# Kernel optimization log

Measured on AMD Instinct MI355X. Metric: run time of the kernel, lower is better.

## Reference

```python
import jax, jax.numpy as jnp
import numpy as np

B, S, D = 8, 2048, 512
EPS = 1e-6
ROPE_THETA = 10000.0


def setup_inputs() -> dict:
    key = jax.random.key(0)
    ks = jax.random.split(key, 8)
    scale = 0.02
    return {
        "x": jax.random.normal(ks[0], (B, S, D), dtype=jnp.float32),
        "conv_w": jax.random.normal(ks[1], (D, D, 3), dtype=jnp.float32) * scale,
        "conv_b": jnp.zeros((D,), dtype=jnp.float32),
        "pre_g": jnp.ones((D,), dtype=jnp.float32),
        "q_g": jnp.ones((D,), dtype=jnp.float32),
        "k_g": jnp.ones((D,), dtype=jnp.float32),
        "Wq": jax.random.normal(ks[2], (D, D), dtype=jnp.float32) * scale,
        "Wk": jax.random.normal(ks[3], (D, D), dtype=jnp.float32) * scale,
        "Wv": jax.random.normal(ks[4], (D, D), dtype=jnp.float32) * scale,
    }


def _rmsnorm(x, g, eps=EPS):
    ms = jnp.mean(jnp.square(x), axis=-1, keepdims=True)
    return x * jax.lax.rsqrt(ms + eps) * g


def _rope_tables(seq_len, head_dim, dtype=jnp.float32):
    inv = 1.0 / (ROPE_THETA ** (jnp.arange(0, head_dim, 2, dtype=dtype) / head_dim))
    freqs = jnp.arange(seq_len, dtype=dtype)[:, None] * inv[None, :]  # [S, D/2]
    return jnp.cos(freqs), jnp.sin(freqs)


def _apply_rope(x, cos, sin):
    # x: [B, S, D]; treat last dim as D/2 complex pairs (interleaved real/imag)
    b, s, d = x.shape
    xr = x.reshape(b, s, d // 2, 2)
    x0, x1 = xr[..., 0], xr[..., 1]
    c = cos[None, :, :]
    sn = sin[None, :, :]
    o0 = x0 * c - x1 * sn
    o1 = x0 * sn + x1 * c
    return jnp.stack([o0, o1], axis=-1).reshape(b, s, d)


def reference(x, conv_w, conv_b, pre_g, q_g, k_g, Wq, Wk, Wv):
    b, s, d = x.shape
    # Conv1d over sequence axis (kernel 3, padding 1)
    xc = jnp.transpose(x, (0, 2, 1))  # [B, D, S]
    xc = jax.lax.conv_general_dilated(
        xc, conv_w, window_strides=(1,), padding=[(1, 1)],
        dimension_numbers=("NCH", "OIH", "NCH"))
    xc = xc + conv_b[None, :, None]
    x_norm = _rmsnorm(jnp.transpose(xc, (0, 2, 1)), pre_g)  # [B, S, D]

    q = _rmsnorm(jnp.einsum("bsd,ed->bse", x_norm, Wq), q_g)
    k = _rmsnorm(jnp.einsum("bsd,ed->bse", x_norm, Wk), k_g)
    v = jnp.einsum("bsd,ed->bse", x_norm, Wv)

    cos, sin = _rope_tables(s, d, x.dtype)
    q = _apply_rope(q, cos, sin)
    k = _apply_rope(k, cos, sin)

    scores = jnp.einsum("bqd,bkd->bqk", q, k) / jnp.sqrt(jnp.asarray(d, x.dtype))
    w = jax.nn.softmax(scores, axis=-1)  # dropout is identity in eval mode
    attended = jnp.einsum("bqk,bkd->bqd", w, v)
    out = x + attended
    return out.mean(axis=1)  # [B, D]
```

## Files before the change

kernel.cpp:

```cpp
#include <hip/hip_runtime.h>
#include <math.h>

#define BB 8
#define SS 2048
#define DDIM 512
#define KC 1536
#define EPSV 1e-6f
#define SCALE 0.044194173824159216f
#define LDP  40
#define LDP2 72

typedef unsigned short ushort_t;
using short8 = __attribute__((ext_vector_type(8))) short;
using f32x4  = __attribute__((ext_vector_type(4))) float;

__device__ inline unsigned short f2bf(float f) {
    union { float f; unsigned int u; } v; v.f = f;
    unsigned int r = v.u + 0x7FFFu + ((v.u >> 16) & 1u);
    return (unsigned short)(r >> 16);
}
__device__ inline unsigned int packbf(float a, float b) {
    return (unsigned int)f2bf(a) | ((unsigned int)f2bf(b) << 16);
}
__device__ inline float bf2f(unsigned short s) {
    union { unsigned int u; float f; } v; v.u = ((unsigned int)s) << 16; return v.f;
}
__device__ inline short8 ldfrag(const ushort_t* s, int row, int ko) {
    return *reinterpret_cast<const short8*>(&s[row * LDP + ko]);
}
__device__ inline short8 ldfrag2(const ushort_t* s, int row, int ko) {
    return *reinterpret_cast<const short8*>(&s[row * LDP2 + ko]);
}
__device__ inline uint4 lda_bc(const ushort_t* Ag, int s_, int ko) {
    return (s_ >= 0 && s_ < SS) ? *reinterpret_cast<const uint4*>(&Ag[(size_t)s_ * DDIM + ko])
                                : make_uint4(0, 0, 0, 0);
}

__global__ __launch_bounds__(256) void kx_cast(const float* __restrict__ x,
                                               ushort_t* __restrict__ xbf,
                                               float* __restrict__ xsum)
{
    const int t = threadIdx.x;
    const int b = blockIdx.y;
    const int r0 = blockIdx.x * 16;
    const int c0 = 2 * t;
    float s0 = 0.f, s1 = 0.f;
    for (int r = 0; r < 16; r++) {
        size_t row = (size_t)b * SS + r0 + r;
        float2 v = *reinterpret_cast<const float2*>(&x[row * DDIM + c0]);
        s0 += v.x; s1 += v.y;
        *reinterpret_cast<unsigned int*>(&xbf[row * DDIM + c0]) = packbf(v.x, v.y);
    }
    atomicAdd(&xsum[b * DDIM + c0], s0);
    atomicAdd(&xsum[b * DDIM + c0 + 1], s1);
}

__global__ __launch_bounds__(256) void k0_prep(
    const float* __restrict__ conv_w, const float* __restrict__ Wq,
    const float* __restrict__ Wk, const float* __restrict__ Wv,
    ushort_t* __restrict__ wcat, ushort_t* __restrict__ wqkv)
{
    int idx = blockIdx.x * 256 + threadIdx.x;
    {
        int o = idx / KC, kk = idx - o * KC;
        int t = kk >> 9, i = kk & 511;
        wcat[idx] = f2bf(conv_w[(size_t)o * KC + i * 3 + t]);
    }
    {
        int n = idx >> 9, d = idx & 511;
        const float* src = (n < 512) ? &Wq[(size_t)n * DDIM + d]
                         : (n < 1024) ? &Wk[(size_t)(n - 512) * DDIM + d]
                         : &Wv[(size_t)(n - 1024) * DDIM + d];
        wqkv[idx] = f2bf(*src);
    }
}

__global__ __launch_bounds__(256) void k1b_conv(
    const ushort_t* __restrict__ xbf, const ushort_t* __restrict__ wcat,
    const float* __restrict__ conv_b, ushort_t* __restrict__ ybf, float* __restrict__ rs)
{
    __shared__ ushort_t As[128 * LDP2];
    __shared__ ushort_t Bs[128 * LDP2];
    const int t = threadIdx.x;
    const int lane = t & 63, w = t >> 6;
    const int lm = lane & 15, lq = lane >> 4;
    const int wm = w >> 1, wn = w & 1;
    const int sr = t >> 3, sc = (t & 7) * 8;
    const int s0 = blockIdx.x * 128;
    const int n0 = blockIdx.y * 128;
    const int b  = blockIdx.z;
    const ushort_t* Ag = xbf + (size_t)b * SS * DDIM;
    const ushort_t* Bg = wcat + (size_t)n0 * KC;

    f32x4 acc[4][4];
    #pragma unroll
    for (int i = 0; i < 4; i++)
        #pragma unroll
        for (int j = 0; j < 4; j++) acc[i][j] = (f32x4){0.f, 0.f, 0.f, 0.f};

    uint4 ra0, ra1, ra2, ra3, rb0, rb1, rb2, rb3;
    #define LOADAB(dc) { \
        int tg_ = (dc) >> 3, ko_ = ((dc) & 7) * 64 + sc, kb_ = (dc) * 64 + sc; \
        int sa_ = s0 + sr + tg_ - 1; \
        ra0 = lda_bc(Ag, sa_,      ko_); ra1 = lda_bc(Ag, sa_ + 32, ko_); \
        ra2 = lda_bc(Ag, sa_ + 64, ko_); ra3 = lda_bc(Ag, sa_ + 96, ko_); \
        rb0 = *reinterpret_cast<const uint4*>(&Bg[(size_t)sr * KC + kb_]); \
        rb1 = *reinterpret_cast<const uint4*>(&Bg[(size_t)(sr + 32) * KC + kb_]); \
        rb2 = *reinterpret_cast<const uint4*>(&Bg[(size_t)(sr + 64) * KC + kb_]); \
        rb3 = *reinterpret_cast<const uint4*>(&Bg[(size_t)(sr + 96) * KC + kb_]); }

    LOADAB(0);
    for (int dc = 0; dc < 24; dc++) {
        *reinterpret_cast<uint4*>(&As[(sr)      * LDP2 + sc]) = ra0;
        *reinterpret_cast<uint4*>(&As[(sr + 32) * LDP2 + sc]) = ra1;
        *reinterpret_cast<uint4*>(&As[(sr + 64) * LDP2 + sc]) = ra2;
        *reinterpret_cast<uint4*>(&As[(sr + 96) * LDP2 + sc]) = ra3;
        *reinterpret_cast<uint4*>(&Bs[(sr)      * LDP2 + sc]) = rb0;
        *reinterpret_cast<uint4*>(&Bs[(sr + 32) * LDP2 + sc]) = rb1;
        *reinterpret_cast<uint4*>(&Bs[(sr + 64) * LDP2 + sc]) = rb2;
        *reinterpret_cast<uint4*>(&Bs[(sr + 96) * LDP2 + sc]) = rb3;
        __syncthreads();
        if (dc < 23) LOADAB(dc + 1);
        #pragma unroll
        for (int half = 0; half < 2; half++) {
            short8 af0 = ldfrag2(As, wm * 64 +  0 + lm, half * 32 + lq * 8);
            short8 af1 = ldfrag2(As, wm * 64 + 16 + lm, half * 32 + lq * 8);
            short8 af2 = ldfrag2(As, wm * 64 + 32 + lm, half * 32 + lq * 8);
            short8 af3 = ldfrag2(As, wm * 64 + 48 + lm, half * 32 + lq * 8);
            #pragma unroll
            for (int nt = 0; nt < 4; nt++) {
                short8 bfv = ldfrag2(Bs, wn * 64 + nt * 16 + lm, half * 32 + lq * 8);
                acc[0][nt] = __builtin_amdgcn_mfma_f32_16x16x32_bf16(af0, bfv, acc[0][nt], 0, 0, 0);
                acc[1][nt] = __builtin_amdgcn_mfma_f32_16x16x32_bf16(af1, bfv, acc[1][nt], 0, 0, 0);
                acc[2][nt] = __builtin_amdgcn_mfma_f32_16x16x32_bf16(af2, bfv, acc[2][nt], 0, 0, 0);
                acc[3][nt] = __builtin_amdgcn_mfma_f32_16x16x32_bf16(af3, bfv, acc[3][nt], 0, 0, 0);
            }
        }
        __syncthreads();
    }
    #undef LOADAB

    const int rbase = s0 + wm * 64;
    const int cbase = n0 + wn * 64;
    ushort_t* yb = ybf + (size_t)b * SS * DDIM;
    float* rsb = rs + (size_t)b * SS;
    float bias[4];
    #pragma unroll
    for (int nt = 0; nt < 4; nt++) bias[nt] = conv_b[cbase + nt * 16 + lm];
    #pragma unroll
    for (int mt = 0; mt < 4; mt++) {
        float pr[4] = {0.f, 0.f, 0.f, 0.f};
        #pragma unroll
        for (int nt = 0; nt < 4; nt++) {
            #pragma unroll
            for (int r = 0; r < 4; r++) {
                float val = acc[mt][nt][r] + bias[nt];
                yb[(size_t)(rbase + mt * 16 + lq * 4 + r) * DDIM + cbase + nt * 16 + lm] = f2bf(val);
                pr[r] = fmaf(val, val, pr[r]);
            }
        }
        #pragma unroll
        for (int r = 0; r < 4; r++) {
            float p = pr[r];
            p += __shfl_xor(p, 1, 64); p += __shfl_xor(p, 2, 64);
            p += __shfl_xor(p, 4, 64); p += __shfl_xor(p, 8, 64);
            if (lm == 0) atomicAdd(&rsb[rbase + mt * 16 + lq * 4 + r], p);
        }
    }
}

__global__ __launch_bounds__(256) void k1n_norm(
    const ushort_t* __restrict__ ybf, const float* __restrict__ rs,
    const float* __restrict__ pre_g, ushort_t* __restrict__ xnbf)
{
    const int t = threadIdx.x;
    const int b = blockIdx.y;
    const int r0 = blockIdx.x * 8;
    float2 pg = *reinterpret_cast<const float2*>(&pre_g[2 * t]);
    for (int r = 0; r < 8; r++) {
        size_t row = (size_t)b * SS + r0 + r;
        float inv = rsqrtf(rs[row] * (1.0f / DDIM) + EPSV);
        unsigned int yv = *reinterpret_cast<const unsigned int*>(&ybf[row * DDIM + 2 * t]);
        float v0 = bf2f((ushort_t)(yv & 0xFFFF)), v1 = bf2f((ushort_t)(yv >> 16));
        *reinterpret_cast<unsigned int*>(&xnbf[row * DDIM + 2 * t]) =
            packbf(v0 * inv * pg.x, v1 * inv * pg.y);
    }
}

__global__ __launch_bounds__(256) void k1c_qkv(
    const ushort_t* __restrict__ xnbf, const ushort_t* __restrict__ wqkv,
    ushort_t* __restrict__ qraw, ushort_t* __restrict__ kraw, ushort_t* __restrict__ vb,
    float* __restrict__ rq, float* __restrict__ rk)
{
    __shared__ ushort_t As[128 * LDP2];
    __shared__ ushort_t Bs[128 * LDP2];
    const int t = threadIdx.x;
    const int lane = t & 63, w = t >> 6;
    const int lm = lane & 15, lq = lane >> 4;
    const int wm = w >> 1, wn = w & 1;
    const int sr = t >> 3, sc = (t & 7) * 8;
    const int s0 = blockIdx.x * 128;
    const int n0 = blockIdx.y * 128;
    const int b  = blockIdx.z;
    const ushort_t* Ag = xnbf + ((size_t)b * SS + s0) * DDIM;
    const ushort_t* Bg = wqkv + (size_t)n0 * DDIM;

    f32x4 acc[4][4];
    #pragma unroll
    for (int i = 0; i < 4; i++)
        #pragma unroll
        for (int j = 0; j < 4; j++) acc[i][j] = (f32x4){0.f, 0.f, 0.f, 0.f};

    uint4 ra0, ra1, ra2, ra3, rb0, rb1, rb2, rb3;
    #define LOADAB2(dc) { \
        int ko_ = (dc) * 64 + sc; \
        ra0 = *reinterpret_cast<const uint4*>(&Ag[(size_t)sr * DDIM + ko_]); \
        ra1 = *reinterpret_cast<const uint4*>(&Ag[(size_t)(sr + 32) * DDIM + ko_]); \
        ra2 = *reinterpret_cast<const uint4*>(&Ag[(size_t)(sr + 64) * DDIM + ko_]); \
        ra3 = *reinterpret_cast<const uint4*>(&Ag[(size_t)(sr + 96) * DDIM + ko_]); \
        rb0 = *reinterpret_cast<const uint4*>(&Bg[(size_t)sr * DDIM + ko_]); \
        rb1 = *reinterpret_cast<const uint4*>(&Bg[(size_t)(sr + 32) * DDIM + ko_]); \
        rb2 = *reinterpret_cast<const uint4*>(&Bg[(size_t)(sr + 64) * DDIM + ko_]); \
        rb3 = *reinterpret_cast<const uint4*>(&Bg[(size_t)(sr + 96) * DDIM + ko_]); }

    LOADAB2(0);
    for (int dc = 0; dc < 8; dc++) {
        *reinterpret_cast<uint4*>(&As[(sr)      * LDP2 + sc]) = ra0;
        *reinterpret_cast<uint4*>(&As[(sr + 32) * LDP2 + sc]) = ra1;
        *reinterpret_cast<uint4*>(&As[(sr + 64) * LDP2 + sc]) = ra2;
        *reinterpret_cast<uint4*>(&As[(sr + 96) * LDP2 + sc]) = ra3;
        *reinterpret_cast<uint4*>(&Bs[(sr)      * LDP2 + sc]) = rb0;
        *reinterpret_cast<uint4*>(&Bs[(sr + 32) * LDP2 + sc]) = rb1;
        *reinterpret_cast<uint4*>(&Bs[(sr + 64) * LDP2 + sc]) = rb2;
        *reinterpret_cast<uint4*>(&Bs[(sr + 96) * LDP2 + sc]) = rb3;
        __syncthreads();
        if (dc < 7) LOADAB2(dc + 1);
        #pragma unroll
        for (int half = 0; half < 2; half++) {
            short8 af0 = ldfrag2(As, wm * 64 +  0 + lm, half * 32 + lq * 8);
            short8 af1 = ldfrag2(As, wm * 64 + 16 + lm, half * 32 + lq * 8);
            short8 af2 = ldfrag2(As, wm * 64 + 32 + lm, half * 32 + lq * 8);
            short8 af3 = ldfrag2(As, wm * 64 + 48 + lm, half * 32 + lq * 8);
            #pragma unroll
            for (int nt = 0; nt < 4; nt++) {
                short8 bfv = ldfrag2(Bs, wn * 64 + nt * 16 + lm, half * 32 + lq * 8);
                acc[0][nt] = __builtin_amdgcn_mfma_f32_16x16x32_bf16(af0, bfv, acc[0][nt], 0, 0, 0);
                acc[1][nt] = __builtin_amdgcn_mfma_f32_16x16x32_bf16(af1, bfv, acc[1][nt], 0, 0, 0);
                acc[2][nt] = __builtin_amdgcn_mfma_f32_16x16x32_bf16(af2, bfv, acc[2][nt], 0, 0, 0);
                acc[3][nt] = __builtin_amdgcn_mfma_f32_16x16x32_bf16(af3, bfv, acc[3][nt], 0, 0, 0);
            }
        }
        __syncthreads();
    }
    #undef LOADAB2

    const int which = blockIdx.y >> 2;
    const int rbase = s0 + wm * 64;
    const int cbase = ((blockIdx.y & 3) * 128) + wn * 64;
    if (which == 2) {
        ushort_t* vbb = vb + (size_t)b * SS * DDIM;
        #pragma unroll
        for (int mt = 0; mt < 4; mt++)
            #pragma unroll
            for (int nt = 0; nt < 4; nt++)
                #pragma unroll
                for (int r = 0; r < 4; r++)
                    vbb[(size_t)(rbase + mt * 16 + lq * 4 + r) * DDIM + cbase + nt * 16 + lm] =
                        f2bf(acc[mt][nt][r]);
    } else {
        ushort_t* db = (which ? kraw : qraw) + (size_t)b * SS * DDIM;
        float* rb = (which ? rk : rq) + (size_t)b * SS;
        #pragma unroll
        for (int mt = 0; mt < 4; mt++) {
            float pr[4] = {0.f, 0.f, 0.f, 0.f};
            #pragma unroll
            for (int nt = 0; nt < 4; nt++) {
                #pragma unroll
                for (int r = 0; r < 4; r++) {
                    float val = acc[mt][nt][r];
                    db[(size_t)(rbase + mt * 16 + lq * 4 + r) * DDIM + cbase + nt * 16 + lm] = f2bf(val);
                    pr[r] = fmaf(val, val, pr[r]);
                }
            }
            #pragma unroll
            for (int r = 0; r < 4; r++) {
                float p = pr[r];
                p += __shfl_xor(p, 1, 64); p += __shfl_xor(p, 2, 64);
                p += __shfl_xor(p, 4, 64); p += __shfl_xor(p, 8, 64);
                if (lm == 0) atomicAdd(&rb[rbase + mt * 16 + lq * 4 + r], p);
            }
        }
    }
}

__global__ __launch_bounds__(256) void k1d_rope(
    ushort_t* q_io, ushort_t* k_io,
    const float* __restrict__ rq, const float* __restrict__ rk,
    const float* __restrict__ q_g, const float* __restrict__ k_g)
{
    const int t = threadIdx.x;
    const int b = blockIdx.y;
    const int r0 = blockIdx.x * 8;
    const int c0 = 2 * t;
    float qg0 = q_g[c0], qg1 = q_g[c0 + 1];
    float kg0 = k_g[c0], kg1 = k_g[c0 + 1];
    float invf = (float)pow(10000.0, -(double)c0 / (double)DDIM);
    for (int r = 0; r < 8; r++) {
        int srow = r0 + r;
        size_t rowi = (size_t)b * SS + srow;
        float iq = rsqrtf(rq[rowi] * (1.0f / DDIM) + EPSV);
        float ik = rsqrtf(rk[rowi] * (1.0f / DDIM) + EPSV);
        size_t off = rowi * DDIM + c0;
        unsigned int qv = *reinterpret_cast<const unsigned int*>(&q_io[off]);
        unsigned int kv = *reinterpret_cast<const unsigned int*>(&k_io[off]);
        float q0 = bf2f((ushort_t)(qv & 0xFFFF)) * iq * qg0;
        float q1 = bf2f((ushort_t)(qv >> 16)) * iq * qg1;
        float k0v = bf2f((ushort_t)(kv & 0xFFFF)) * ik * kg0;
        float k1v = bf2f((ushort_t)(kv >> 16)) * ik * kg1;
        float ang = (float)srow * invf, sn, cs;
        sincosf(ang, &sn, &cs);
        *reinterpret_cast<unsigned int*>(&q_io[off]) = packbf(q0 * cs - q1 * sn, q0 * sn + q1 * cs);
        *reinterpret_cast<unsigned int*>(&k_io[off]) = packbf(k0v * cs - k1v * sn, k0v * sn + k1v * cs);
    }
}

__global__ __launch_bounds__(256, 4) void k2a_rowsum(
    const ushort_t* __restrict__ qb, const ushort_t* __restrict__ kb,
    ushort_t* __restrict__ P, float* __restrict__ l)
{
    __shared__ ushort_t As[128 * LDP];
    __shared__ ushort_t Bs[128 * LDP];
    const int t = threadIdx.x;
    const int lane = t & 63, w = t >> 6;
    const int lm = lane & 15, lq = lane >> 4;
    const int wm = w >> 1, wn = w & 1;
    const int srow = t >> 2, scol = (t & 3) * 8;
    const int b  = blockIdx.x;
    const int qt = blockIdx.y;
    const int kt = blockIdx.z;

    const ushort_t* Ag = qb + ((size_t)b * SS + qt * 128) * DDIM;
    const ushort_t* Bg = kb + ((size_t)b * SS + kt * 128) * DDIM;

    f32x4 acc[4][4];
    #pragma unroll
    for (int i = 0; i < 4; i++)
        #pragma unroll
        for (int j = 0; j < 4; j++) acc[i][j] = (f32x4){0.f, 0.f, 0.f, 0.f};

    uint4 ra0 = *reinterpret_cast<const uint4*>(&Ag[(size_t)srow * DDIM + scol]);
    uint4 ra1 = *reinterpret_cast<const uint4*>(&Ag[(size_t)(srow + 64) * DDIM + scol]);
    uint4 rb0 = *reinterpret_cast<const uint4*>(&Bg[(size_t)srow * DDIM + scol]);
    uint4 rb1 = *reinterpret_cast<const uint4*>(&Bg[(size_t)(srow + 64) * DDIM + scol]);

    for (int dc = 0; dc < 16; dc++) {
        *reinterpret_cast<uint4*>(&As[srow * LDP + scol]) = ra0;
        *reinterpret_cast<uint4*>(&As[(srow + 64) * LDP + scol]) = ra1;
        *reinterpret_cast<uint4*>(&Bs[srow * LDP + scol]) = rb0;
        *reinterpret_cast<uint4*>(&Bs[(srow + 64) * LDP + scol]) = rb1;
        __syncthreads();
        if (dc < 15) {
            int off = (dc + 1) * 32 + scol;
            ra0 = *reinterpret_cast<const uint4*>(&Ag[(size_t)srow * DDIM + off]);
            ra1 = *reinterpret_cast<const uint4*>(&Ag[(size_t)(srow + 64) * DDIM + off]);
            rb0 = *reinterpret_cast<const uint4*>(&Bg[(size_t)srow * DDIM + off]);
            rb1 = *reinterpret_cast<const uint4*>(&Bg[(size_t)(srow + 64) * DDIM + off]);
        }
        short8 af[4];
        #pragma unroll
        for (int mt = 0; mt < 4; mt++)
            af[mt] = ldfrag(As, wm * 64 + mt * 16 + lm, lq * 8);
        #pragma unroll
        for (int nt = 0; nt < 4; nt++) {
            short8 bfv = ldfrag(Bs, wn * 64 + nt * 16 + lm, lq * 8);
            #pragma unroll
            for (int mt = 0; mt < 4; mt++)
                acc[mt][nt] = __builtin_amdgcn_mfma_f32_16x16x32_bf16(af[mt], bfv, acc[mt][nt], 0, 0, 0);
        }
        __syncthreads();
    }

    const int rbase = qt * 128 + wm * 64;
    const int cbase = kt * 128 + wn * 64;
    ushort_t* Pb = P + (size_t)b * SS * SS;
    float* lrow = l + (size_t)b * SS;
    #pragma unroll
    for (int mt = 0; mt < 4; mt++) {
        #pragma unroll
        for (int r = 0; r < 4; r++) {
            const int row = rbase + mt * 16 + lq * 4 + r;
            float rowp = 0.f;
            #pragma unroll
            for (int nt = 0; nt < 4; nt++) {
                float e = __expf(acc[mt][nt][r] * SCALE);
                Pb[(size_t)row * SS + cbase + nt * 16 + lm] = f2bf(e);
                rowp += e;
            }
            float p = rowp;
            p += __shfl_xor(p, 1, 64); p += __shfl_xor(p, 2, 64);
            p += __shfl_xor(p, 4, 64); p += __shfl_xor(p, 8, 64);
            if (lm == 0) atomicAdd(&lrow[row], p);
        }
    }
}

__global__ __launch_bounds__(256) void k2c_colred(
    const ushort_t* __restrict__ P, const float* __restrict__ l,
    float* __restrict__ cw)
{
    const int t = threadIdx.x;
    const int b = blockIdx.z;
    const int k0 = blockIdx.x * 1024 + t * 4;
    const int q0 = blockIdx.y * 128;
    const ushort_t* Pb = P + ((size_t)b * SS + q0) * SS;
    const float* lb = l + (size_t)b * SS + q0;
    float a0 = 0.f, a1 = 0.f, a2 = 0.f, a3 = 0.f;
    for (int q = 0; q < 128; q++) {
        float rl = 1.0f / lb[q];
        uint2 pp = *reinterpret_cast<const uint2*>(&Pb[(size_t)q * SS + k0]);
        a0 = fmaf(bf2f((ushort_t)(pp.x & 0xFFFF)), rl, a0);
        a1 = fmaf(bf2f((ushort_t)(pp.x >> 16)), rl, a1);
        a2 = fmaf(bf2f((ushort_t)(pp.y & 0xFFFF)), rl, a2);
        a3 = fmaf(bf2f((ushort_t)(pp.y >> 16)), rl, a3);
    }
    atomicAdd(&cw[(size_t)b * SS + k0], a0);
    atomicAdd(&cw[(size_t)b * SS + k0 + 1], a1);
    atomicAdd(&cw[(size_t)b * SS + k0 + 2], a2);
    atomicAdd(&cw[(size_t)b * SS + k0 + 3], a3);
}

__global__ __launch_bounds__(256) void k4_out(
    const float* __restrict__ xsum, const ushort_t* __restrict__ v,
    const float* __restrict__ cwv, float* __restrict__ out)
{
    const int b = blockIdx.x, c = blockIdx.y;
    const int t = threadIdx.x;
    const int srow0 = c * (SS / 16);
    const ushort_t* vb = v + ((size_t)b * SS + srow0) * DDIM;
    const float* cwb   = cwv + (size_t)b * SS + srow0;
    float a0 = (c == 0) ? xsum[b * DDIM + t]       : 0.f;
    float a1 = (c == 0) ? xsum[b * DDIM + t + 256] : 0.f;
    for (int r = 0; r < SS / 16; r++) {
        float w = cwb[r];
        a0 += w * bf2f(vb[(size_t)r * DDIM + t]);
        a1 += w * bf2f(vb[(size_t)r * DDIM + t + 256]);
    }
    atomicAdd(&out[b * DDIM + t],       a0 * (1.0f / SS));
    atomicAdd(&out[b * DDIM + t + 256], a1 * (1.0f / SS));
}

extern "C" void kernel_launch(void* const* d_in, const int* in_sizes, int n_in,
                              void* d_out, int out_size, void* d_ws, size_t ws_size,
                              hipStream_t stream)
{
    const float* x      = (const float*)d_in[0];
    const float* conv_w = (const float*)d_in[1];
    const float* conv_b = (const float*)d_in[2];
    const float* pre_g  = (const float*)d_in[3];
    const float* q_g    = (const float*)d_in[4];
    const float* k_g    = (const float*)d_in[5];
    const float* Wq     = (const float*)d_in[6];
    const float* Wk     = (const float*)d_in[7];
    const float* Wv     = (const float*)d_in[8];
    float* out          = (float*)d_out;

    const size_t NTOK = (size_t)BB * SS * DDIM;
    char* p = (char*)d_ws;
    ushort_t* xbf = (ushort_t*)p; p += NTOK * 2;
    ushort_t* ybf = (ushort_t*)p; p += NTOK * 2;
    ushort_t* xn  = (ushort_t*)p; p += NTOK * 2;
                         p += NTOK * 2;
    ushort_t* qio = (ushort_t*)p; p += NTOK * 2;
    ushort_t* kio = (ushort_t*)p; p += NTOK * 2;
    ushort_t* vb  = (ushort_t*)p; p += NTOK * 2;
    ushort_t* wcat = (ushort_t*)p; p += (size_t)DDIM * KC * 2;
    ushort_t* wqkv = (ushort_t*)p; p += (size_t)KC * DDIM * 2;
    float* rs   = (float*)p; p += (size_t)BB * SS * 4;
    float* rq   = (float*)p; p += (size_t)BB * SS * 4;
    float* rk   = (float*)p; p += (size_t)BB * SS * 4;
    float* lbuf = (float*)p; p += (size_t)BB * SS * 4;
    float* cwb  = (float*)p; p += (size_t)BB * SS * 4;
    float* xsum = (float*)p; p += (size_t)BB * DDIM * 4;

    ushort_t* Pbuf = xbf;

    (void)hipMemsetAsync(d_out, 0, (size_t)out_size * sizeof(float), stream);
    (void)hipMemsetAsync(rs, 0, ((size_t)BB * SS * 5 + (size_t)BB * DDIM) * sizeof(float), stream);

    kx_cast<<<dim3(SS / 16, BB), 256, 0, stream>>>(x, xbf, xsum);
    k0_prep<<<dim3(DDIM * KC / 256), 256, 0, stream>>>(conv_w, Wq, Wk, Wv, wcat, wqkv);
    k1b_conv<<<dim3(SS / 128, 4, BB), 256, 0, stream>>>(xbf, wcat, conv_b, ybf, rs);
    k1n_norm<<<dim3(SS / 8, BB), 256, 0, stream>>>(ybf, rs, pre_g, xn);
    k1c_qkv<<<dim3(SS / 128, 12, BB), 256, 0, stream>>>(xn, wqkv, qio, kio, vb, rq, rk);
    k1d_rope<<<dim3(SS / 8, BB), 256, 0, stream>>>(qio, kio, rq, rk, q_g, k_g);
    k2a_rowsum<<<dim3(BB, SS / 128, SS / 128), 256, 0, stream>>>(qio, kio, Pbuf, lbuf);
    k2c_colred<<<dim3(SS / 1024, SS / 128, BB), 256, 0, stream>>>(Pbuf, lbuf, cwb);
    k4_out<<<dim3(BB, 16), 256, 0, stream>>>(xsum, vb, cwb, out);
}
```

Measured before the change: 287.4 us.

## Use direct global-to-LDS loads with XOR-swizzled shared tiles in GEMM kernels

The conv, QKV and score GEMM kernels now move tiles straight from global memory into LDS with global_load_lds, replacing the register staging and padded LDS rows. The LDS layout is XOR-swizzled to avoid bank conflicts without padding. The bf16 copy of x gets zero halo rows, so the conv's shifted-row loads need no bounds checks and map onto one contiguous address. The score kernel also widens its K step to 64 and drops its occupancy launch hint. The aim is to cut register pressure and staging instructions, but the register prefetch that overlapped loads with MFMA work is gone, so each iteration now waits on its loads.

```diff
diff --git a/kernel.cpp b/kernel.cpp
--- a/kernel.cpp
+++ b/kernel.cpp
@@ -3,12 +3,11 @@
 
 #define BB 8
 #define SS 2048
+#define SSG 2050
 #define DDIM 512
 #define KC 1536
 #define EPSV 1e-6f
 #define SCALE 0.044194173824159216f
-#define LDP  40
-#define LDP2 72
 
 typedef unsigned short ushort_t;
 using short8 = __attribute__((ext_vector_type(8))) short;
@@ -25,15 +24,15 @@
 __device__ inline float bf2f(unsigned short s) {
     union { unsigned int u; float f; } v; v.u = ((unsigned int)s) << 16; return v.f;
 }
-__device__ inline short8 ldfrag(const ushort_t* s, int row, int ko) {
-    return *reinterpret_cast<const short8*>(&s[row * LDP + ko]);
-}
-__device__ inline short8 ldfrag2(const ushort_t* s, int row, int ko) {
-    return *reinterpret_cast<const short8*>(&s[row * LDP2 + ko]);
-}
-__device__ inline uint4 lda_bc(const ushort_t* Ag, int s_, int ko) {
-    return (s_ >= 0 && s_ < SS) ? *reinterpret_cast<const uint4*>(&Ag[(size_t)s_ * DDIM + ko])
-                                : make_uint4(0, 0, 0, 0);
+
+__device__ inline void gload16(const ushort_t* g, ushort_t* l) {
+    __builtin_amdgcn_global_load_lds(
+        (__attribute__((address_space(1))) const void*)g,
+        (__attribute__((address_space(3))) void*)l, 16, 0, 0);
+}
+
+__device__ inline short8 ldswz(const ushort_t* s, int row, int c) {
+    return *reinterpret_cast<const short8*>(&s[(row << 6) + ((c ^ (row & 7)) << 3)]);
 }
 
 __global__ __launch_bounds__(256) void kx_cast(const float* __restrict__ x,
@@ -44,12 +43,17 @@
     const int b = blockIdx.y;
     const int r0 = blockIdx.x * 16;
     const int c0 = 2 * t;
+    if (blockIdx.x == 0) {
+        *reinterpret_cast<unsigned int*>(&xbf[((size_t)b * SSG) * DDIM + c0]) = 0u;
+        *reinterpret_cast<unsigned int*>(&xbf[((size_t)b * SSG + SS + 1) * DDIM + c0]) = 0u;
+    }
     float s0 = 0.f, s1 = 0.f;
     for (int r = 0; r < 16; r++) {
-        size_t row = (size_t)b * SS + r0 + r;
-        float2 v = *reinterpret_cast<const float2*>(&x[row * DDIM + c0]);
+        size_t srow = (size_t)b * SS + r0 + r;
+        size_t drow = (size_t)b * SSG + 1 + r0 + r;
+        float2 v = *reinterpret_cast<const float2*>(&x[srow * DDIM + c0]);
         s0 += v.x; s1 += v.y;
-        *reinterpret_cast<unsigned int*>(&xbf[row * DDIM + c0]) = packbf(v.x, v.y);
+        *reinterpret_cast<unsigned int*>(&xbf[drow * DDIM + c0]) = packbf(v.x, v.y);
     }
     atomicAdd(&xsum[b * DDIM + c0], s0);
     atomicAdd(&xsum[b * DDIM + c0 + 1], s1);
@@ -79,66 +83,63 @@
     const ushort_t* __restrict__ xbf, const ushort_t* __restrict__ wcat,
     const float* __restrict__ conv_b, ushort_t* __restrict__ ybf, float* __restrict__ rs)
 {
-    __shared__ ushort_t As[128 * LDP2];
-    __shared__ ushort_t Bs[128 * LDP2];
+    __shared__ alignas(16) ushort_t As[128 * 64];
+    __shared__ alignas(16) ushort_t Bs[128 * 64];
     const int t = threadIdx.x;
     const int lane = t & 63, w = t >> 6;
     const int lm = lane & 15, lq = lane >> 4;
     const int wm = w >> 1, wn = w & 1;
-    const int sr = t >> 3, sc = (t & 7) * 8;
+    const int lr = lane >> 3;
+    const int lc = ((lane & 7) ^ lr) << 3;
     const int s0 = blockIdx.x * 128;
     const int n0 = blockIdx.y * 128;
     const int b  = blockIdx.z;
-    const ushort_t* Ag = xbf + (size_t)b * SS * DDIM;
+    const ushort_t* Ag = xbf + (size_t)b * SSG * DDIM;
     const ushort_t* Bg = wcat + (size_t)n0 * KC;
 
+    const ushort_t* pa[4]; const ushort_t* pb[4];
+    ushort_t* da[4]; ushort_t* db[4];
+    #pragma unroll
+    for (int i = 0; i < 4; i++) {
+        const int tr = (w * 4 + i) * 8 + lr;
+        pa[i] = &Ag[(size_t)(s0 + tr) * DDIM + lc];
+        pb[i] = &Bg[(size_t)tr * KC + lc];
+        da[i] = &As[(w * 4 + i) * 512];
+        db[i] = &Bs[(w * 4 + i) * 512];
+    }
+
     f32x4 acc[4][4];
     #pragma unroll
     for (int i = 0; i < 4; i++)
         #pragma unroll
         for (int j = 0; j < 4; j++) acc[i][j] = (f32x4){0.f, 0.f, 0.f, 0.f};
 
-    uint4 ra0, ra1, ra2, ra3, rb0, rb1, rb2, rb3;
-    #define LOADAB(dc) { \
-        int tg_ = (dc) >> 3, ko_ = ((dc) & 7) * 64 + sc, kb_ = (dc) * 64 + sc; \
-        int sa_ = s0 + sr + tg_ - 1; \
-        ra0 = lda_bc(Ag, sa_,      ko_); ra1 = lda_bc(Ag, sa_ + 32, ko_); \
-        ra2 = lda_bc(Ag, sa_ + 64, ko_); ra3 = lda_bc(Ag, sa_ + 96, ko_); \
-        rb0 = *reinterpret_cast<const uint4*>(&Bg[(size_t)sr * KC + kb_]); \
-        rb1 = *reinterpret_cast<const uint4*>(&Bg[(size_t)(sr + 32) * KC + kb_]); \
-        rb2 = *reinterpret_cast<const uint4*>(&Bg[(size_t)(sr + 64) * KC + kb_]); \
-        rb3 = *reinterpret_cast<const uint4*>(&Bg[(size_t)(sr + 96) * KC + kb_]); }
-
-    LOADAB(0);
     for (int dc = 0; dc < 24; dc++) {
-        *reinterpret_cast<uint4*>(&As[(sr)      * LDP2 + sc]) = ra0;
-        *reinterpret_cast<uint4*>(&As[(sr + 32) * LDP2 + sc]) = ra1;
-        *reinterpret_cast<uint4*>(&As[(sr + 64) * LDP2 + sc]) = ra2;
-        *reinterpret_cast<uint4*>(&As[(sr + 96) * LDP2 + sc]) = ra3;
-        *reinterpret_cast<uint4*>(&Bs[(sr)      * LDP2 + sc]) = rb0;
-        *reinterpret_cast<uint4*>(&Bs[(sr + 32) * LDP2 + sc]) = rb1;
-        *reinterpret_cast<uint4*>(&Bs[(sr + 64) * LDP2 + sc]) = rb2;
-        *reinterpret_cast<uint4*>(&Bs[(sr + 96) * LDP2 + sc]) = rb3;
         __syncthreads();
-        if (dc < 23) LOADAB(dc + 1);
+        const int koff = dc * 64;
+        #pragma unroll
+        for (int i = 0; i < 4; i++) {
+            gload16(pa[i] + koff, da[i]);
+            gload16(pb[i] + koff, db[i]);
+        }
+        __syncthreads();
         #pragma unroll
         for (int half = 0; half < 2; half++) {
-            short8 af0 = ldfrag2(As, wm * 64 +  0 + lm, half * 32 + lq * 8);
-            short8 af1 = ldfrag2(As, wm * 64 + 16 + lm, half * 32 + lq * 8);
-            short8 af2 = ldfrag2(As, wm * 64 + 32 + lm, half * 32 + lq * 8);
-            short8 af3 = ldfrag2(As, wm * 64 + 48 + lm, half * 32 + lq * 8);
+            const int cb = (half << 2) | lq;
+            short8 af0 = ldswz(As, wm * 64 +  0 + lm, cb);
+            short8 af1 = ldswz(As, wm * 64 + 16 + lm, cb);
+            short8 af2 = ldswz(As, wm * 64 + 32 + lm, cb);
+            short8 af3 = ldswz(As, wm * 64 + 48 + lm, cb);
             #pragma unroll
             for (int nt = 0; nt < 4; nt++) {
-                short8 bfv = ldfrag2(Bs, wn * 64 + nt * 16 + lm, half * 32 + lq * 8);
+                short8 bfv = ldswz(Bs, wn * 64 + nt * 16 + lm, cb);
                 acc[0][nt] = __builtin_amdgcn_mfma_f32_16x16x32_bf16(af0, bfv, acc[0][nt], 0, 0, 0);
                 acc[1][nt] = __builtin_amdgcn_mfma_f32_16x16x32_bf16(af1, bfv, acc[1][nt], 0, 0, 0);
                 acc[2][nt] = __builtin_amdgcn_mfma_f32_16x16x32_bf16(af2, bfv, acc[2][nt], 0, 0, 0);
                 acc[3][nt] = __builtin_amdgcn_mfma_f32_16x16x32_bf16(af3, bfv, acc[3][nt], 0, 0, 0);
             }
         }
-        __syncthreads();
-    }
-    #undef LOADAB
+    }
 
     const int rbase = s0 + wm * 64;
     const int cbase = n0 + wn * 64;
@@ -192,67 +193,63 @@
     ushort_t* __restrict__ qraw, ushort_t* __restrict__ kraw, ushort_t* __restrict__ vb,
     float* __restrict__ rq, float* __restrict__ rk)
 {
-    __shared__ ushort_t As[128 * LDP2];
-    __shared__ ushort_t Bs[128 * LDP2];
+    __shared__ alignas(16) ushort_t As[128 * 64];
+    __shared__ alignas(16) ushort_t Bs[128 * 64];
     const int t = threadIdx.x;
     const int lane = t & 63, w = t >> 6;
     const int lm = lane & 15, lq = lane >> 4;
     const int wm = w >> 1, wn = w & 1;
-    const int sr = t >> 3, sc = (t & 7) * 8;
+    const int lr = lane >> 3;
+    const int lc = ((lane & 7) ^ lr) << 3;
     const int s0 = blockIdx.x * 128;
     const int n0 = blockIdx.y * 128;
     const int b  = blockIdx.z;
     const ushort_t* Ag = xnbf + ((size_t)b * SS + s0) * DDIM;
     const ushort_t* Bg = wqkv + (size_t)n0 * DDIM;
 
+    const ushort_t* pa[4]; const ushort_t* pb[4];
+    ushort_t* da[4]; ushort_t* db[4];
+    #pragma unroll
+    for (int i = 0; i < 4; i++) {
+        const int tr = (w * 4 + i) * 8 + lr;
+        pa[i] = &Ag[(size_t)tr * DDIM + lc];
+        pb[i] = &Bg[(size_t)tr * DDIM + lc];
+        da[i] = &As[(w * 4 + i) * 512];
+        db[i] = &Bs[(w * 4 + i) * 512];
+    }
+
     f32x4 acc[4][4];
     #pragma unroll
     for (int i = 0; i < 4; i++)
         #pragma unroll
         for (int j = 0; j < 4; j++) acc[i][j] = (f32x4){0.f, 0.f, 0.f, 0.f};
 
-    uint4 ra0, ra1, ra2, ra3, rb0, rb1, rb2, rb3;
-    #define LOADAB2(dc) { \
-        int ko_ = (dc) * 64 + sc; \
-        ra0 = *reinterpret_cast<const uint4*>(&Ag[(size_t)sr * DDIM + ko_]); \
-        ra1 = *reinterpret_cast<const uint4*>(&Ag[(size_t)(sr + 32) * DDIM + ko_]); \
-        ra2 = *reinterpret_cast<const uint4*>(&Ag[(size_t)(sr + 64) * DDIM + ko_]); \
-        ra3 = *reinterpret_cast<const uint4*>(&Ag[(size_t)(sr + 96) * DDIM + ko_]); \
-        rb0 = *reinterpret_cast<const uint4*>(&Bg[(size_t)sr * DDIM + ko_]); \
-        rb1 = *reinterpret_cast<const uint4*>(&Bg[(size_t)(sr + 32) * DDIM + ko_]); \
-        rb2 = *reinterpret_cast<const uint4*>(&Bg[(size_t)(sr + 64) * DDIM + ko_]); \
-        rb3 = *reinterpret_cast<const uint4*>(&Bg[(size_t)(sr + 96) * DDIM + ko_]); }
-
-    LOADAB2(0);
     for (int dc = 0; dc < 8; dc++) {
-        *reinterpret_cast<uint4*>(&As[(sr)      * LDP2 + sc]) = ra0;
-        *reinterpret_cast<uint4*>(&As[(sr + 32) * LDP2 + sc]) = ra1;
-        *reinterpret_cast<uint4*>(&As[(sr + 64) * LDP2 + sc]) = ra2;
-        *reinterpret_cast<uint4*>(&As[(sr + 96) * LDP2 + sc]) = ra3;
-        *reinterpret_cast<uint4*>(&Bs[(sr)      * LDP2 + sc]) = rb0;
-        *reinterpret_cast<uint4*>(&Bs[(sr + 32) * LDP2 + sc]) = rb1;
-        *reinterpret_cast<uint4*>(&Bs[(sr + 64) * LDP2 + sc]) = rb2;
-        *reinterpret_cast<uint4*>(&Bs[(sr + 96) * LDP2 + sc]) = rb3;
         __syncthreads();
-        if (dc < 7) LOADAB2(dc + 1);
+        const int koff = dc * 64;
+        #pragma unroll
+        for (int i = 0; i < 4; i++) {
+            gload16(pa[i] + koff, da[i]);
+            gload16(pb[i] + koff, db[i]);
+        }
+        __syncthreads();
         #pragma unroll
         for (int half = 0; half < 2; half++) {
-            short8 af0 = ldfrag2(As, wm * 64 +  0 + lm, half * 32 + lq * 8);
-            short8 af1 = ldfrag2(As, wm * 64 + 16 + lm, half * 32 + lq * 8);
-            short8 af2 = ldfrag2(As, wm * 64 + 32 + lm, half * 32 + lq * 8);
-            short8 af3 = ldfrag2(As, wm * 64 + 48 + lm, half * 32 + lq * 8);
+            const int cb = (half << 2) | lq;
+            short8 af0 = ldswz(As, wm * 64 +  0 + lm, cb);
+            short8 af1 = ldswz(As, wm * 64 + 16 + lm, cb);
+            short8 af2 = ldswz(As, wm * 64 + 32 + lm, cb);
+            short8 af3 = ldswz(As, wm * 64 + 48 + lm, cb);
             #pragma unroll
             for (int nt = 0; nt < 4; nt++) {
-                short8 bfv = ldfrag2(Bs, wn * 64 + nt * 16 + lm, half * 32 + lq * 8);
+                short8 bfv = ldswz(Bs, wn * 64 + nt * 16 + lm, cb);
                 acc[0][nt] = __builtin_amdgcn_mfma_f32_16x16x32_bf16(af0, bfv, acc[0][nt], 0, 0, 0);
                 acc[1][nt] = __builtin_amdgcn_mfma_f32_16x16x32_bf16(af1, bfv, acc[1][nt], 0, 0, 0);
                 acc[2][nt] = __builtin_amdgcn_mfma_f32_16x16x32_bf16(af2, bfv, acc[2][nt], 0, 0, 0);
                 acc[3][nt] = __builtin_amdgcn_mfma_f32_16x16x32_bf16(af3, bfv, acc[3][nt], 0, 0, 0);
             }
         }
-        __syncthreads();
-    }
-    #undef LOADAB2
+    }
 
     const int which = blockIdx.y >> 2;
     const int rbase = s0 + wm * 64;
@@ -268,7 +265,7 @@
                     vbb[(size_t)(rbase + mt * 16 + lq * 4 + r) * DDIM + cbase + nt * 16 + lm] =
                         f2bf(acc[mt][nt][r]);
     } else {
-        ushort_t* db = (which ? kraw : qraw) + (size_t)b * SS * DDIM;
+        ushort_t* db2 = (which ? kraw : qraw) + (size_t)b * SS * DDIM;
         float* rb = (which ? rk : rq) + (size_t)b * SS;
         #pragma unroll
         for (int mt = 0; mt < 4; mt++) {
@@ -278,7 +275,7 @@
                 #pragma unroll
                 for (int r = 0; r < 4; r++) {
                     float val = acc[mt][nt][r];
-                    db[(size_t)(rbase + mt * 16 + lq * 4 + r) * DDIM + cbase + nt * 16 + lm] = f2bf(val);
+                    db2[(size_t)(rbase + mt * 16 + lq * 4 + r) * DDIM + cbase + nt * 16 + lm] = f2bf(val);
                     pr[r] = fmaf(val, val, pr[r]);
                 }
             }
@@ -324,60 +321,66 @@
     }
 }
 
-__global__ __launch_bounds__(256, 4) void k2a_rowsum(
+__global__ __launch_bounds__(256) void k2a_rowsum(
     const ushort_t* __restrict__ qb, const ushort_t* __restrict__ kb,
     ushort_t* __restrict__ P, float* __restrict__ l)
 {
-    __shared__ ushort_t As[128 * LDP];
-    __shared__ ushort_t Bs[128 * LDP];
+    __shared__ alignas(16) ushort_t As[128 * 64];
+    __shared__ alignas(16) ushort_t Bs[128 * 64];
     const int t = threadIdx.x;
     const int lane = t & 63, w = t >> 6;
     const int lm = lane & 15, lq = lane >> 4;
     const int wm = w >> 1, wn = w & 1;
-    const int srow = t >> 2, scol = (t & 3) * 8;
+    const int lr = lane >> 3;
+    const int lc = ((lane & 7) ^ lr) << 3;
     const int b  = blockIdx.x;
     const int qt = blockIdx.y;
     const int kt = blockIdx.z;
-
     const ushort_t* Ag = qb + ((size_t)b * SS + qt * 128) * DDIM;
     const ushort_t* Bg = kb + ((size_t)b * SS + kt * 128) * DDIM;
 
+    const ushort_t* pa[4]; const ushort_t* pb[4];
+    ushort_t* da[4]; ushort_t* db[4];
+    #pragma unroll
+    for (int i = 0; i < 4; i++) {
+        const int tr = (w * 4 + i) * 8 + lr;
+        pa[i] = &Ag[(size_t)tr * DDIM + lc];
+        pb[i] = &Bg[(size_t)tr * DDIM + lc];
+        da[i] = &As[(w * 4 + i) * 512];
+        db[i] = &Bs[(w * 4 + i) * 512];
+    }
+
     f32x4 acc[4][4];
     #pragma unroll
     for (int i = 0; i < 4; i++)
         #pragma unroll
         for (int j = 0; j < 4; j++) acc[i][j] = (f32x4){0.f, 0.f, 0.f, 0.f};
 
-    uint4 ra0 = *reinterpret_cast<const uint4*>(&Ag[(size_t)srow * DDIM + scol]);
-    uint4 ra1 = *reinterpret_cast<const uint4*>(&Ag[(size_t)(srow + 64) * DDIM + scol]);
-    uint4 rb0 = *reinterpret_cast<const uint4*>(&Bg[(size_t)srow * DDIM + scol]);
-    uint4 rb1 = *reinterpret_cast<const uint4*>(&Bg[(size_t)(srow + 64) * DDIM + scol]);
-
-    for (int dc = 0; dc < 16; dc++) {
-        *reinterpret_cast<uint4*>(&As[srow * LDP + scol]) = ra0;
-        *reinterpret_cast<uint4*>(&As[(srow + 64) * LDP + scol]) = ra1;
-        *reinterpret_cast<uint4*>(&Bs[srow * LDP + scol]) = rb0;
-        *reinterpret_cast<uint4*>(&Bs[(srow + 64) * LDP + scol]) = rb1;
+    for (int dc = 0; dc < 8; dc++) {
         __syncthreads();
-        if (dc < 15) {
-            int off = (dc + 1) * 32 + scol;
-            ra0 = *reinterpret_cast<const uint4*>(&Ag[(size_t)srow * DDIM + off]);
-            ra1 = *reinterpret_cast<const uint4*>(&Ag[(size_t)(srow + 64) * DDIM + off]);
-            rb0 = *reinterpret_cast<const uint4*>(&Bg[(size_t)srow * DDIM + off]);
-            rb1 = *reinterpret_cast<const uint4*>(&Bg[(size_t)(srow + 64) * DDIM + off]);
-        }
-        short8 af[4];
-        #pragma unroll
-        for (int mt = 0; mt < 4; mt++)
-            af[mt] = ldfrag(As, wm * 64 + mt * 16 + lm, lq * 8);
-        #pragma unroll
-        for (int nt = 0; nt < 4; nt++) {
-            short8 bfv = ldfrag(Bs, wn * 64 + nt * 16 + lm, lq * 8);
-            #pragma unroll
-            for (int mt = 0; mt < 4; mt++)
-                acc[mt][nt] = __builtin_amdgcn_mfma_f32_16x16x32_bf16(af[mt], bfv, acc[mt][nt], 0, 0, 0);
+        const int koff = dc * 64;
+        #pragma unroll
+        for (int i = 0; i < 4; i++) {
+            gload16(pa[i] + koff, da[i]);
+            gload16(pb[i] + koff, db[i]);
         }
         __syncthreads();
+        #pragma unroll
+        for (int half = 0; half < 2; half++) {
+            const int cb = (half << 2) | lq;
+            short8 af0 = ldswz(As, wm * 64 +  0 + lm, cb);
+            short8 af1 = ldswz(As, wm * 64 + 16 + lm, cb);
+            short8 af2 = ldswz(As, wm * 64 + 32 + lm, cb);
+            short8 af3 = ldswz(As, wm * 64 + 48 + lm, cb);
+            #pragma unroll
+            for (int nt = 0; nt < 4; nt++) {
+                short8 bfv = ldswz(Bs, wn * 64 + nt * 16 + lm, cb);
+                acc[0][nt] = __builtin_amdgcn_mfma_f32_16x16x32_bf16(af0, bfv, acc[0][nt], 0, 0, 0);
+                acc[1][nt] = __builtin_amdgcn_mfma_f32_16x16x32_bf16(af1, bfv, acc[1][nt], 0, 0, 0);
+                acc[2][nt] = __builtin_amdgcn_mfma_f32_16x16x32_bf16(af2, bfv, acc[2][nt], 0, 0, 0);
+                acc[3][nt] = __builtin_amdgcn_mfma_f32_16x16x32_bf16(af3, bfv, acc[3][nt], 0, 0, 0);
+            }
+        }
     }
 
     const int rbase = qt * 128 + wm * 64;
@@ -464,9 +467,10 @@
     const float* Wv     = (const float*)d_in[8];
     float* out          = (float*)d_out;
 
-    const size_t NTOK = (size_t)BB * SS * DDIM;
+    const size_t NTOK  = (size_t)BB * SS * DDIM;
+    const size_t NTOKG = (size_t)BB * SSG * DDIM;
     char* p = (char*)d_ws;
-    ushort_t* xbf = (ushort_t*)p; p += NTOK * 2;
+    ushort_t* xbf = (ushort_t*)p; p += NTOKG * 2;
     ushort_t* ybf = (ushort_t*)p; p += NTOK * 2;
     ushort_t* xn  = (ushort_t*)p; p += NTOK * 2;
                          p += NTOK * 2;
```

After: 273.4 us. 4.9% less time.
